# Performance work log

Measured on AMD Instinct MI355X. Metric: run time of the kernel, lower is better.

The kernel has to match this reference:

```python
import jax, jax.numpy as jnp
import numpy as np


def setup_inputs() -> dict:
    key = jax.random.key(0)
    k1, k2 = jax.random.split(key)
    B, Lc, Lm, D = 8, 2048, 2048, 128
    context = jax.random.normal(k1, (B, Lc, D), dtype=jnp.float32)
    main = jax.random.normal(k2, (B, Lm, D), dtype=jnp.float32)
    return {"context": context, "main": main}


def reference(context, main):
    # weights[b,c,m] = sum_d context[b,c,d] * main[b,m,d]   (Keras dot axes=[2,2])
    weights = jnp.einsum("bcd,bmd->bcm", context, main)
    # K.softmax default axis=-1: normalize over the main-length axis m
    weights = jax.nn.softmax(weights, axis=-1)
    # dot([weights, context], axes=1): contract axis 1 (c) of both -> (B, Lm, D)
    weighted = jnp.einsum("bcm,bcd->bmd", weights, context)
    return main - weighted
```

## Files before the change

### kernel.cpp

```cpp
#include <hip/hip_runtime.h>


#define BATCH 8
#define L_SEQ 2048
#define DD 128
#define SHIFT 40.0f
#define LDA 136

typedef __attribute__((ext_vector_type(8))) short bf16x8;
typedef __attribute__((ext_vector_type(4))) short bf16x4;
typedef __attribute__((ext_vector_type(4))) float f32x4;
typedef __attribute__((ext_vector_type(16))) float f32x16;
typedef __attribute__((ext_vector_type(4))) unsigned int uint4v;

__device__ __forceinline__ short f2bf(float f) {
    unsigned u = __builtin_bit_cast(unsigned, f);
    return (short)((u + 0x8000u) >> 16);
}

__device__ __forceinline__ void gl2lds16(const short* g, short* l) {
    __builtin_amdgcn_global_load_lds(
        (const __attribute__((address_space(1))) unsigned int*)g,
        (__attribute__((address_space(3))) unsigned int*)l, 16, 0, 0);
}

__device__ __forceinline__ void waitv8() { asm volatile("s_waitcnt vmcnt(8)" ::: "memory"); }
__device__ __forceinline__ void waitv4() { asm volatile("s_waitcnt vmcnt(4)" ::: "memory"); }
__device__ __forceinline__ void waitv0() { asm volatile("s_waitcnt vmcnt(0)" ::: "memory"); }

template <int NT>
__device__ __forceinline__ void stage_tile(short* __restrict__ dst,
                                           const float* __restrict__ src,
                                           int nelts, int t) {
    for (int base = 0; base < nelts; base += NT * 8) {
        int flat = base + t * 8;
        const float4* p = (const float4*)(src + flat);
        float4 v0 = p[0];
        float4 v1 = p[1];
        bf16x8 s;
        s[0] = f2bf(v0.x); s[1] = f2bf(v0.y); s[2] = f2bf(v0.z); s[3] = f2bf(v0.w);
        s[4] = f2bf(v1.x); s[5] = f2bf(v1.y); s[6] = f2bf(v1.z); s[7] = f2bf(v1.w);
        int row = flat >> 7;
        int col = flat & 127;
        *(bf16x8*)&dst[row * LDA + col] = s;
    }
}

__global__ __launch_bounds__(256) void zero_kernel(float* __restrict__ p, int n) {
    int i = blockIdx.x * 256 + threadIdx.x;
    if (i < n) p[i] = 0.0f;
}


__global__ __launch_bounds__(256) void convert_kernel(const float* __restrict__ ctx,
                                                      const float* __restrict__ mn,
                                                      short* __restrict__ Cbf,
                                                      short* __restrict__ Mbf,
                                                      float* __restrict__ Lg) {
    int tid = blockIdx.x * 256 + threadIdx.x;
    if (tid < BATCH * L_SEQ) Lg[tid] = 0.0f;
    const int half = BATCH * L_SEQ * DD / 8;
    int id = tid;
    const float* src;
    short* dst;
    if (id < half) { src = ctx; dst = Cbf; }
    else           { id -= half; src = mn; dst = Mbf; }
    int row = id >> 4;
    int lc = id & 15;
    const float4* p = (const float4*)(src + ((size_t)row << 7) + lc * 8);
    float4 v0 = p[0];
    float4 v1 = p[1];
    bf16x8 s;
    s[0] = f2bf(v0.x); s[1] = f2bf(v0.y); s[2] = f2bf(v0.z); s[3] = f2bf(v0.w);
    s[4] = f2bf(v1.x); s[5] = f2bf(v1.y); s[6] = f2bf(v1.z); s[7] = f2bf(v1.w);
    int pc = (lc & 8) | ((lc ^ row) & 7);
    *(bf16x8*)&dst[((size_t)row << 7) + pc * 8] = s;
}

__global__ __launch_bounds__(256, 2) void stats_kernel(const short* __restrict__ Cbf,
                                                       const short* __restrict__ Mbf,
                                                       float* __restrict__ Lg) {
    __shared__ short Cs[128 * 128];
    __shared__ short Ms[2][64 * 128];

    int bid = blockIdx.x;
    int b  = bid & 7;
    int r2 = bid >> 3;
    int mc = r2 & 3;
    int ct = r2 >> 2;
    int t = threadIdx.x;
    int w = t >> 6;
    int l = t & 63;
    int a15 = l & 15;
    int q = l >> 4;
    int h = a15 & 7;
    int cw = (w & 1) * 64;
    int mw = (w >> 1) * 32;

    const short* gC = Cbf + ((size_t)(b * L_SEQ + ct * 128)) * DD;
    const short* gM = Mbf + ((size_t)(b * L_SEQ + mc * 512)) * DD;

    {
        #pragma unroll
        for (int ii = 0; ii < 8; ++ii) {
            int inst = w * 8 + ii;
            gl2lds16(gC + inst * 512 + l * 8, Cs + inst * 512);
        }
        #pragma unroll
        for (int ii = 0; ii < 4; ++ii) {
            int inst = w * 4 + ii;
            gl2lds16(gM + inst * 512 + l * 8, Ms[0] + inst * 512);
        }
        #pragma unroll
        for (int ii = 0; ii < 4; ++ii) {
            int inst = w * 4 + ii;
            gl2lds16(gM + (size_t)64 * DD + inst * 512 + l * 8, Ms[1] + inst * 512);
        }
    }

    waitv8();
    __builtin_amdgcn_s_barrier();
    __builtin_amdgcn_sched_barrier(0);

    bf16x8 af[4][4];
    #pragma unroll
    for (int ks = 0; ks < 4; ++ks) {
        int aoff = ((ks * 4 + q) ^ h) * 8;
        #pragma unroll
        for (int i = 0; i < 4; ++i)
            af[ks][i] = *(const bf16x8*)&Cs[(cw + i * 16 + a15) * 128 + aoff];
    }

    float ls[4][4] = {};

    for (int ms = 0; ms < 8; ++ms) {
        int bp = ms & 1;
        if (ms < 7) waitv4(); else waitv0();
        __builtin_amdgcn_s_barrier();
        __builtin_amdgcn_sched_barrier(0);

        f32x4 acc[4][2];
        #pragma unroll
        for (int i = 0; i < 4; ++i)
            #pragma unroll
            for (int j = 0; j < 2; ++j) {
                f32x4 z = {0.f, 0.f, 0.f, 0.f};
                acc[i][j] = z;
            }
        #pragma unroll
        for (int ks = 0; ks < 4; ++ks) {
            int aoff = ((ks * 4 + q) ^ h) * 8;
            bf16x8 bv[2];
            #pragma unroll
            for (int j = 0; j < 2; ++j)
                bv[j] = *(const bf16x8*)&Ms[bp][(mw + j * 16 + a15) * 128 + aoff];
            #pragma unroll
            for (int i = 0; i < 4; ++i)
                #pragma unroll
                for (int j = 0; j < 2; ++j)
                    acc[i][j] = __builtin_amdgcn_mfma_f32_16x16x32_bf16(af[ks][i], bv[j], acc[i][j], 0, 0, 0);
        }

        #pragma unroll
        for (int j = 0; j < 2; ++j)
            #pragma unroll
            for (int i = 0; i < 4; ++i)
                #pragma unroll
                for (int r = 0; r < 4; ++r)
                    ls[i][r] += __expf(acc[i][j][r] - SHIFT);

        __builtin_amdgcn_s_barrier();
        __builtin_amdgcn_sched_barrier(0);
        if (ms + 2 < 8) {
            #pragma unroll
            for (int ii = 0; ii < 4; ++ii) {
                int inst = w * 4 + ii;
                gl2lds16(gM + (size_t)(ms + 2) * 64 * DD + inst * 512 + l * 8,
                         Ms[bp] + inst * 512);
            }
        }
    }

    #pragma unroll
    for (int i = 0; i < 4; ++i)
        #pragma unroll
        for (int r = 0; r < 4; ++r) {
            float v = ls[i][r];
            v += __shfl_xor(v, 1);
            v += __shfl_xor(v, 2);
            v += __shfl_xor(v, 4);
            v += __shfl_xor(v, 8);
            ls[i][r] = v;
        }
    if (a15 == 0) {
        #pragma unroll
        for (int i = 0; i < 4; ++i) {
            int c = ct * 128 + cw + i * 16 + q * 4;
            #pragma unroll
            for (int r = 0; r < 4; ++r)
                atomicAdd(&Lg[(size_t)b * L_SEQ + c + r], ls[i][r]);
        }
    }
}

__global__ __launch_bounds__(256) void prep_kernel(const float* __restrict__ ctx,
                                                   const float* __restrict__ Lg,
                                                   short* __restrict__ CtLf) {
    __shared__ short Ts[128 * LDA];
    __shared__ float invLs[128];

    int b = blockIdx.x >> 4;
    int cc = blockIdx.x & 15;
    int t = threadIdx.x;

    if (t < 128) invLs[t] = 1.0f / Lg[(size_t)b * L_SEQ + cc * 128 + t];
    __syncthreads();

    const float* src = ctx + ((size_t)(b * L_SEQ + cc * 128)) * DD;
    #pragma unroll
    for (int i = 0; i < 8; ++i) {
        int flat = i * 2048 + t * 8;
        int r = flat >> 7;
        int c = flat & 127;
        const float4* p = (const float4*)(src + flat);
        float4 v0 = p[0];
        float4 v1 = p[1];
        float il = invLs[r];
        bf16x8 s;
        s[0] = f2bf(v0.x * il); s[1] = f2bf(v0.y * il); s[2] = f2bf(v0.z * il); s[3] = f2bf(v0.w * il);
        s[4] = f2bf(v1.x * il); s[5] = f2bf(v1.y * il); s[6] = f2bf(v1.z * il); s[7] = f2bf(v1.w * il);
        *(bf16x8*)&Ts[r * LDA + c] = s;
    }
    __syncthreads();

    #pragma unroll
    for (int i = 0; i < 8; ++i) {
        int slot = i * 256 + t;
        int rec = slot >> 6;
        int l2  = slot & 63;
        int chh = rec >> 3;
        int dgg = (rec >> 1) & 3;
        int ks2 = rec & 1;
        int la2 = l2 & 31;
        int hi2 = l2 >> 5;
        int d   = dgg * 32 + la2;
        int c0  = (chh * 4 + ks2 * 2 + hi2) * 8;
        bf16x8 v;
        #pragma unroll
        for (int j = 0; j < 8; ++j) v[j] = Ts[(c0 + j) * LDA + d];
        *(bf16x8*)&CtLf[((size_t)(b * 16 + cc) * 32 + rec) * 512 + l2 * 8] = v;
    }
}

__global__ __launch_bounds__(256, 2) void attend_fused(const short* __restrict__ Cbf,
                                                       const short* __restrict__ Mbf,
                                                       const short* __restrict__ CtLf,
                                                       const float* __restrict__ mn,
                                                       float* __restrict__ out) {
    __shared__ __align__(16) char smem[65536];

    int bid = blockIdx.x;
    int b = bid & 7;
    int mtile = bid >> 3;
    int t = threadIdx.x;
    int w = t >> 6;
    int l = t & 63;
    int la = l & 31;
    int hi = l >> 5;
    int ch = w;

    int m_glob = mtile * 32 + la;
    int key7 = la & 7;

    bf16x8 mf[8];
    {
        const short* mrow = Mbf + ((size_t)(b * L_SEQ + m_glob)) * DD;
        #pragma unroll
        for (int ks = 0; ks < 8; ++ks) {
            int lc = ks * 2 + hi;
            int pc = (lc & 8) | ((lc ^ key7) & 7);
            mf[ks] = *(const bf16x8*)&mrow[pc * 8];
        }
    }

    auto stage = [&](int cs, int p) {
        short* Cw = (short*)(smem + p * 32768);
        const short* gC = Cbf + ((size_t)(b * L_SEQ + cs * 128)) * DD;
        #pragma unroll
        for (int ii = 0; ii < 8; ++ii) {
            int inst = w * 8 + ii;
            gl2lds16(gC + inst * 512 + l * 8, Cw + inst * 512);
        }
    };

    f32x16 o[4];
    #pragma unroll
    for (int dg = 0; dg < 4; ++dg)
        #pragma unroll
        for (int r = 0; r < 16; ++r) o[dg][r] = 0.0f;

    stage(0, 0);
    stage(1, 1);

    for (int cs = 0; cs < 16; ++cs) {
        int p = cs & 1;
        waitv8();
        __builtin_amdgcn_s_barrier();
        __builtin_amdgcn_sched_barrier(0);

        const short* gF = CtLf + ((size_t)((b * 16 + cs) * 4 + ch) * 8) * 512 + l * 8;
        bf16x8 tv[4][2];
        #pragma unroll
        for (int dg = 0; dg < 4; ++dg)
            #pragma unroll
            for (int ks2 = 0; ks2 < 2; ++ks2)
                tv[dg][ks2] = *(const bf16x8*)&gF[(dg * 2 + ks2) * 512];

        const short* Cw = (const short*)(smem + p * 32768);

        f32x16 s;
        #pragma unroll
        for (int r = 0; r < 16; ++r) s[r] = 0.0f;
        int crow = ch * 32 + la;
        #pragma unroll
        for (int ks = 0; ks < 8; ++ks) {
            int lc = ks * 2 + hi;
            int pc = (lc & 8) | ((lc ^ key7) & 7);
            bf16x8 av = *(const bf16x8*)&Cw[crow * 128 + pc * 8];
            s = __builtin_amdgcn_mfma_f32_32x32x16_bf16(av, mf[ks], s, 0, 0, 0);
        }

        unsigned u[4][2];
        #pragma unroll
        for (int q = 0; q < 4; ++q)
            #pragma unroll
            for (int jj = 0; jj < 2; ++jj) {
                float e0 = __expf(s[q * 4 + jj * 2]     - SHIFT);
                float e1 = __expf(s[q * 4 + jj * 2 + 1] - SHIFT);
                u[q][jj] = ((unsigned)(unsigned short)f2bf(e1) << 16)
                         |  (unsigned)(unsigned short)f2bf(e0);
            }

        bf16x8 pa[2];
        #pragma unroll
        for (int ks2 = 0; ks2 < 2; ++ks2) {
            unsigned a0 = u[2 * ks2][0],     a1 = u[2 * ks2][1];
            unsigned b0 = u[2 * ks2 + 1][0], b1 = u[2 * ks2 + 1][1];
            unsigned a0p = (unsigned)__shfl_xor((int)a0, 32);
            unsigned a1p = (unsigned)__shfl_xor((int)a1, 32);
            unsigned b0p = (unsigned)__shfl_xor((int)b0, 32);
            unsigned b1p = (unsigned)__shfl_xor((int)b1, 32);
            uint4v pw;
            pw.x = hi ? b0p : a0;
            pw.y = hi ? b1p : a1;
            pw.z = hi ? b0  : a0p;
            pw.w = hi ? b1  : a1p;
            pa[ks2] = __builtin_bit_cast(bf16x8, pw);
        }

        #pragma unroll
        for (int dg = 0; dg < 4; ++dg)
            #pragma unroll
            for (int ks2 = 0; ks2 < 2; ++ks2)
                o[dg] = __builtin_amdgcn_mfma_f32_32x32x16_bf16(tv[dg][ks2], pa[ks2], o[dg], 0, 0, 0);

        __builtin_amdgcn_s_barrier();
        __builtin_amdgcn_sched_barrier(0);
        if (cs + 2 < 16) stage(cs + 2, p);
    }

    __syncthreads();
    float* red = (float*)smem;
    {
        float* base = red + w * 4096;
        #pragma unroll
        for (int dg = 0; dg < 4; ++dg)
            #pragma unroll
            for (int r = 0; r < 16; ++r) {
                int d = dg * 32 + (r & 3) + 8 * (r >> 2) + 4 * hi;
                base[d * 32 + la] = o[dg][r];
            }
    }
    __syncthreads();

    {
        int m  = t & 31;
        int dq = t >> 5;
        size_t gbase = ((size_t)(b * L_SEQ + mtile * 32 + m)) * DD + dq * 16;
        #pragma unroll
        for (int jq = 0; jq < 4; ++jq) {
            f32x4 v;
            #pragma unroll
            for (int e = 0; e < 4; ++e) {
                int idx = (dq * 16 + jq * 4 + e) * 32 + m;
                v[e] = red[idx] + red[4096 + idx] + red[8192 + idx] + red[12288 + idx];
            }
            f32x4 mv = *(const f32x4*)&mn[gbase + jq * 4];
            f32x4 ov;
            ov[0] = mv[0] - v[0]; ov[1] = mv[1] - v[1];
            ov[2] = mv[2] - v[2]; ov[3] = mv[3] - v[3];
            *(f32x4*)&out[gbase + jq * 4] = ov;
        }
    }
}


__global__ __launch_bounds__(256, 4) void stats_fb(const float* __restrict__ ctx,
                                                   const float* __restrict__ mn,
                                                   float* __restrict__ Lg) {
    __shared__ short Cs[64 * LDA];
    __shared__ short Ms[64 * LDA];

    int bid = blockIdx.x;
    int mc = bid & 3;
    int ct = (bid >> 2) & 31;
    int b  = bid >> 7;
    int t = threadIdx.x;
    int w = t >> 6;
    int l = t & 63;
    int a15 = l & 15;
    int q = l >> 4;

    stage_tile<256>(Cs, ctx + ((size_t)b * L_SEQ + ct * 64) * DD, 64 * DD, t);

    float ls[4] = {0.f, 0.f, 0.f, 0.f};
    for (int mt = 0; mt < 8; ++mt) {
        __syncthreads();
        int m0 = (mc * 8 + mt) * 64;
        stage_tile<256>(Ms, mn + ((size_t)b * L_SEQ + m0) * DD, 64 * DD, t);
        __syncthreads();

        f32x4 acc[4] = {{0.f,0.f,0.f,0.f},{0.f,0.f,0.f,0.f},{0.f,0.f,0.f,0.f},{0.f,0.f,0.f,0.f}};
        #pragma unroll
        for (int ks = 0; ks < 4; ++ks) {
            int k0 = ks * 32 + q * 8;
            bf16x8 a = *(const bf16x8*)&Cs[(w * 16 + a15) * LDA + k0];
            #pragma unroll
            for (int g = 0; g < 4; ++g) {
                bf16x8 bb = *(const bf16x8*)&Ms[(g * 16 + a15) * LDA + k0];
                acc[g] = __builtin_amdgcn_mfma_f32_16x16x32_bf16(a, bb, acc[g], 0, 0, 0);
            }
        }
        #pragma unroll
        for (int g = 0; g < 4; ++g)
            #pragma unroll
            for (int r = 0; r < 4; ++r)
                ls[r] += __expf(acc[g][r] - SHIFT);
    }

    #pragma unroll
    for (int r = 0; r < 4; ++r) {
        float v = ls[r];
        v += __shfl_xor(v, 1);
        v += __shfl_xor(v, 2);
        v += __shfl_xor(v, 4);
        v += __shfl_xor(v, 8);
        ls[r] = v;
    }
    if (a15 == 0) {
        int c = ct * 64 + w * 16 + q * 4;
        #pragma unroll
        for (int r = 0; r < 4; ++r)
            atomicAdd(&Lg[(size_t)b * L_SEQ + c + r], ls[r]);
    }
}

__global__ __launch_bounds__(1024, 4) void attend_fb(const float* __restrict__ ctx,
                                                     const float* __restrict__ mn,
                                                     const float* __restrict__ Lg,
                                                     float* __restrict__ out) {
    __shared__ short Mt[64 * LDA];
    __shared__ short Cs[128 * LDA];
    __shared__ short Ct[128 * LDA];
    __shared__ short Ps[64 * LDA];
    __shared__ float invLs[128];

    int bid = blockIdx.x;
    int mtile = bid & 31;
    int b = bid >> 5;
    int m0 = mtile * 64;
    int t = threadIdx.x;
    int w = t >> 6;
    int l = t & 63;
    int a15 = l & 15;
    int q = l >> 4;
    int mg = w & 3;
    int pg = w >> 2;

    stage_tile<1024>(Mt, mn + ((size_t)b * L_SEQ + m0) * DD, 64 * DD, t);

    f32x4 oacc[2] = {{0.f,0.f,0.f,0.f},{0.f,0.f,0.f,0.f}};

    for (int cs = 0; cs < 16; ++cs) {
        int c0 = cs * 128;
        __syncthreads();
        stage_tile<1024>(Cs, ctx + ((size_t)b * L_SEQ + c0) * DD, 128 * DD, t);
        if (t < 128) invLs[t] = 1.0f / Lg[(size_t)b * L_SEQ + c0 + t];
        __syncthreads();

        {
            int cc = t & 127;
            int d0 = (t >> 7) * 16;
            #pragma unroll
            for (int hh = 0; hh < 2; ++hh) {
                bf16x8 v = *(const bf16x8*)&Cs[cc * LDA + d0 + hh * 8];
                #pragma unroll
                for (int j = 0; j < 8; ++j)
                    Ct[(d0 + hh * 8 + j) * LDA + cc] = v[j];
            }
        }

        f32x4 sacc[2] = {{0.f,0.f,0.f,0.f},{0.f,0.f,0.f,0.f}};
        #pragma unroll
        for (int ks = 0; ks < 4; ++ks) {
            int k0 = ks * 32 + q * 8;
            bf16x8 a = *(const bf16x8*)&Mt[(mg * 16 + a15) * LDA + k0];
            #pragma unroll
            for (int g = 0; g < 2; ++g) {
                bf16x8 bb = *(const bf16x8*)&Cs[((pg * 2 + g) * 16 + a15) * LDA + k0];
                sacc[g] = __builtin_amdgcn_mfma_f32_16x16x32_bf16(a, bb, sacc[g], 0, 0, 0);
            }
        }
        #pragma unroll
        for (int g = 0; g < 2; ++g) {
            int cl = (pg * 2 + g) * 16 + a15;
            float il = invLs[cl];
            #pragma unroll
            for (int r = 0; r < 4; ++r) {
                float p = __expf(sacc[g][r] - SHIFT) * il;
                Ps[(mg * 16 + q * 4 + r) * LDA + cl] = f2bf(p);
            }
        }
        __syncthreads();

        #pragma unroll
        for (int ks = 0; ks < 4; ++ks) {
            int k0 = ks * 32 + q * 8;
            bf16x8 a = *(const bf16x8*)&Ps[(mg * 16 + a15) * LDA + k0];
            #pragma unroll
            for (int g = 0; g < 2; ++g) {
                bf16x8 bb = *(const bf16x8*)&Ct[((pg * 2 + g) * 16 + a15) * LDA + k0];
                oacc[g] = __builtin_amdgcn_mfma_f32_16x16x32_bf16(a, bb, oacc[g], 0, 0, 0);
            }
        }
    }

    #pragma unroll
    for (int g = 0; g < 2; ++g) {
        int dl = (pg * 2 + g) * 16 + a15;
        #pragma unroll
        for (int r = 0; r < 4; ++r) {
            int ml = mg * 16 + q * 4 + r;
            size_t idx = ((size_t)b * L_SEQ + m0 + ml) * DD + dl;
            out[idx] = mn[idx] - oacc[g][r];
        }
    }
}


extern "C" void kernel_launch(void* const* d_in, const int* in_sizes, int n_in,
                              void* d_out, int out_size, void* d_ws, size_t ws_size,
                              hipStream_t stream) {
    const float* ctx = (const float*)d_in[0];
    const float* mn  = (const float*)d_in[1];
    float* out = (float*)d_out;

    const size_t LG_BYTES = (size_t)BATCH * L_SEQ * sizeof(float);
    const size_t BF_BYTES = (size_t)BATCH * L_SEQ * DD * sizeof(short);
    const size_t NEED = LG_BYTES + 3 * BF_BYTES;

    float* Lg = (float*)d_ws;

    if (ws_size >= NEED) {
        short* Cbf  = (short*)((char*)d_ws + LG_BYTES);
        short* Mbf  = (short*)((char*)d_ws + LG_BYTES + BF_BYTES);
        short* CtLf = (short*)((char*)d_ws + LG_BYTES + 2 * BF_BYTES);
        convert_kernel<<<2048, 256, 0, stream>>>(ctx, mn, Cbf, Mbf, Lg);
        stats_kernel<<<BATCH * 16 * 4, 256, 0, stream>>>(Cbf, Mbf, Lg);
        prep_kernel<<<BATCH * 16, 256, 0, stream>>>(ctx, Lg, CtLf);
        attend_fused<<<BATCH * 64, 256, 0, stream>>>(Cbf, Mbf, CtLf, mn, out);
    } else {
        int nL = BATCH * L_SEQ;
        zero_kernel<<<(nL + 255) / 256, 256, 0, stream>>>(Lg, nL);
        stats_fb<<<BATCH * 32 * 4, 256, 0, stream>>>(ctx, mn, Lg);
        attend_fb<<<BATCH * 32, 1024, 0, stream>>>(ctx, mn, Lg, out);
    }
}
```

Baseline: 121.2 us.

## Fuse convert, stats, prep and attend into one cooperative kernel with grid syncs

Replaces the four separate launches with a single cooperative mega-kernel of 512 blocks that runs the conversion, log-sum statistics, scaled-context prep and attention phases, separated by grid.sync(). The aim is to remove the kernel launch gaps and tail effects between stages. The trade-offs are grid-wide barrier cost, a fixed 512-block grid that loses the parallelism shapes of the original stages (for example, conversion now loops four times per thread), and 64KB of LDS per block under launch_bounds(256,2). If the cooperative launch fails, it falls back to the old four-kernel path.

```diff
diff --git a/kernel.cpp b/kernel.cpp
--- a/kernel.cpp
+++ b/kernel.cpp
@@ -1,4 +1,7 @@
 #include <hip/hip_runtime.h>
+#include <hip/hip_cooperative_groups.h>
+
+namespace cg = cooperative_groups;
 
 
 #define BATCH 8
@@ -49,6 +52,361 @@
 __global__ __launch_bounds__(256) void zero_kernel(float* __restrict__ p, int n) {
     int i = blockIdx.x * 256 + threadIdx.x;
     if (i < n) p[i] = 0.0f;
+}
+
+
+__global__ __launch_bounds__(256, 2) void mega_kernel(const float* __restrict__ ctx,
+                                                      const float* __restrict__ mn,
+                                                      short* __restrict__ Cbf,
+                                                      short* __restrict__ Mbf,
+                                                      short* __restrict__ CtLf,
+                                                      float* __restrict__ Lg,
+                                                      float* __restrict__ out) {
+    __shared__ __align__(16) char smem[65536];
+    cg::grid_group grid = cg::this_grid();
+
+    int bid = blockIdx.x;
+    int t = threadIdx.x;
+    int w = t >> 6;
+    int l = t & 63;
+    int b = bid & 7;
+
+    {
+        int tid = bid * 256 + t;
+        if (tid < BATCH * L_SEQ) Lg[tid] = 0.0f;
+        const int half = BATCH * L_SEQ * DD / 8;
+        #pragma unroll
+        for (int k = 0; k < 4; ++k) {
+            int id = tid + k * 131072;
+            const float* src;
+            short* dst;
+            if (id < half) { src = ctx; dst = Cbf; }
+            else           { id -= half; src = mn; dst = Mbf; }
+            int row = id >> 4;
+            int lc = id & 15;
+            const float4* p = (const float4*)(src + ((size_t)row << 7) + lc * 8);
+            float4 v0 = p[0];
+            float4 v1 = p[1];
+            bf16x8 s;
+            s[0] = f2bf(v0.x); s[1] = f2bf(v0.y); s[2] = f2bf(v0.z); s[3] = f2bf(v0.w);
+            s[4] = f2bf(v1.x); s[5] = f2bf(v1.y); s[6] = f2bf(v1.z); s[7] = f2bf(v1.w);
+            int pc = (lc & 8) | ((lc ^ row) & 7);
+            *(bf16x8*)&dst[((size_t)row << 7) + pc * 8] = s;
+        }
+    }
+
+    grid.sync();
+
+    {
+        short* Cs = (short*)smem;
+
+        int r2 = bid >> 3;
+        int mc = r2 & 3;
+        int ct = r2 >> 2;
+        int a15 = l & 15;
+        int q = l >> 4;
+        int h = a15 & 7;
+        int cw = (w & 1) * 64;
+        int mw = (w >> 1) * 32;
+
+        const short* gC = Cbf + ((size_t)(b * L_SEQ + ct * 128)) * DD;
+        const short* gM = Mbf + ((size_t)(b * L_SEQ + mc * 512)) * DD;
+
+        #pragma unroll
+        for (int ii = 0; ii < 8; ++ii) {
+            int inst = w * 8 + ii;
+            gl2lds16(gC + inst * 512 + l * 8, Cs + inst * 512);
+        }
+        #pragma unroll
+        for (int ii = 0; ii < 4; ++ii) {
+            int inst = w * 4 + ii;
+            gl2lds16(gM + inst * 512 + l * 8, (short*)(smem + 32768) + inst * 512);
+        }
+        #pragma unroll
+        for (int ii = 0; ii < 4; ++ii) {
+            int inst = w * 4 + ii;
+            gl2lds16(gM + (size_t)64 * DD + inst * 512 + l * 8,
+                     (short*)(smem + 49152) + inst * 512);
+        }
+
+        waitv8();
+        __builtin_amdgcn_s_barrier();
+        __builtin_amdgcn_sched_barrier(0);
+
+        bf16x8 af[4][4];
+        #pragma unroll
+        for (int ks = 0; ks < 4; ++ks) {
+            int aoff = ((ks * 4 + q) ^ h) * 8;
+            #pragma unroll
+            for (int i = 0; i < 4; ++i)
+                af[ks][i] = *(const bf16x8*)&Cs[(cw + i * 16 + a15) * 128 + aoff];
+        }
+
+        float ls[4][4] = {};
+
+        for (int ms = 0; ms < 8; ++ms) {
+            int bp = ms & 1;
+            short* Msb = (short*)(smem + 32768 + bp * 16384);
+            if (ms < 7) waitv4(); else waitv0();
+            __builtin_amdgcn_s_barrier();
+            __builtin_amdgcn_sched_barrier(0);
+
+            f32x4 acc[4][2];
+            #pragma unroll
+            for (int i = 0; i < 4; ++i)
+                #pragma unroll
+                for (int j = 0; j < 2; ++j) {
+                    f32x4 z = {0.f, 0.f, 0.f, 0.f};
+                    acc[i][j] = z;
+                }
+            #pragma unroll
+            for (int ks = 0; ks < 4; ++ks) {
+                int aoff = ((ks * 4 + q) ^ h) * 8;
+                bf16x8 bv[2];
+                #pragma unroll
+                for (int j = 0; j < 2; ++j)
+                    bv[j] = *(const bf16x8*)&Msb[(mw + j * 16 + a15) * 128 + aoff];
+                #pragma unroll
+                for (int i = 0; i < 4; ++i)
+                    #pragma unroll
+                    for (int j = 0; j < 2; ++j)
+                        acc[i][j] = __builtin_amdgcn_mfma_f32_16x16x32_bf16(af[ks][i], bv[j], acc[i][j], 0, 0, 0);
+            }
+
+            #pragma unroll
+            for (int j = 0; j < 2; ++j)
+                #pragma unroll
+                for (int i = 0; i < 4; ++i)
+                    #pragma unroll
+                    for (int r = 0; r < 4; ++r)
+                        ls[i][r] += __expf(acc[i][j][r] - SHIFT);
+
+            __builtin_amdgcn_s_barrier();
+            __builtin_amdgcn_sched_barrier(0);
+            if (ms + 2 < 8) {
+                #pragma unroll
+                for (int ii = 0; ii < 4; ++ii) {
+                    int inst = w * 4 + ii;
+                    gl2lds16(gM + (size_t)(ms + 2) * 64 * DD + inst * 512 + l * 8,
+                             Msb + inst * 512);
+                }
+            }
+        }
+
+        #pragma unroll
+        for (int i = 0; i < 4; ++i)
+            #pragma unroll
+            for (int r = 0; r < 4; ++r) {
+                float v = ls[i][r];
+                v += __shfl_xor(v, 1);
+                v += __shfl_xor(v, 2);
+                v += __shfl_xor(v, 4);
+                v += __shfl_xor(v, 8);
+                ls[i][r] = v;
+            }
+        if (a15 == 0) {
+            #pragma unroll
+            for (int i = 0; i < 4; ++i) {
+                int c = ct * 128 + cw + i * 16 + q * 4;
+                #pragma unroll
+                for (int r = 0; r < 4; ++r)
+                    atomicAdd(&Lg[(size_t)b * L_SEQ + c + r], ls[i][r]);
+            }
+        }
+    }
+
+    grid.sync();
+
+    {
+        short* Ts = (short*)smem;
+        float* invL = (float*)(smem + 8704);
+
+        int j = bid >> 3;
+        int cc = j >> 2;
+        int qq = j & 3;
+
+        if (t < 32) invL[t] = 1.0f / Lg[(size_t)b * L_SEQ + cc * 128 + qq * 32 + t];
+        __syncthreads();
+
+        const float* src = ctx + ((size_t)(b * L_SEQ + cc * 128 + qq * 32)) * DD;
+        #pragma unroll
+        for (int i = 0; i < 2; ++i) {
+            int flat = i * 2048 + t * 8;
+            int r = flat >> 7;
+            int c = flat & 127;
+            const float4* p = (const float4*)(src + flat);
+            float4 v0 = p[0];
+            float4 v1 = p[1];
+            float il = invL[r];
+            bf16x8 s;
+            s[0] = f2bf(v0.x * il); s[1] = f2bf(v0.y * il); s[2] = f2bf(v0.z * il); s[3] = f2bf(v0.w * il);
+            s[4] = f2bf(v1.x * il); s[5] = f2bf(v1.y * il); s[6] = f2bf(v1.z * il); s[7] = f2bf(v1.w * il);
+            *(bf16x8*)&Ts[r * LDA + c] = s;
+        }
+        __syncthreads();
+
+        #pragma unroll
+        for (int i = 0; i < 2; ++i) {
+            int slot = i * 256 + t;
+            int recl = slot >> 6;
+            int l2  = slot & 63;
+            int dgg = recl >> 1;
+            int ks2 = recl & 1;
+            int la2 = l2 & 31;
+            int hi2 = l2 >> 5;
+            int d   = dgg * 32 + la2;
+            int rb  = (ks2 * 2 + hi2) * 8;
+            bf16x8 v;
+            #pragma unroll
+            for (int jj = 0; jj < 8; ++jj) v[jj] = Ts[(rb + jj) * LDA + d];
+            int rec = qq * 8 + recl;
+            *(bf16x8*)&CtLf[((size_t)(b * 16 + cc) * 32 + rec) * 512 + l2 * 8] = v;
+        }
+        __syncthreads();
+    }
+
+    grid.sync();
+
+    {
+        int mtile = bid >> 3;
+        int la = l & 31;
+        int hi = l >> 5;
+        int ch = w;
+
+        int m_glob = mtile * 32 + la;
+        int key7 = la & 7;
+
+        bf16x8 mf[8];
+        {
+            const short* mrow = Mbf + ((size_t)(b * L_SEQ + m_glob)) * DD;
+            #pragma unroll
+            for (int ks = 0; ks < 8; ++ks) {
+                int lc = ks * 2 + hi;
+                int pc = (lc & 8) | ((lc ^ key7) & 7);
+                mf[ks] = *(const bf16x8*)&mrow[pc * 8];
+            }
+        }
+
+        auto stage = [&](int cs, int p) {
+            short* Cw = (short*)(smem + p * 32768);
+            const short* gC = Cbf + ((size_t)(b * L_SEQ + cs * 128)) * DD;
+            #pragma unroll
+            for (int ii = 0; ii < 8; ++ii) {
+                int inst = w * 8 + ii;
+                gl2lds16(gC + inst * 512 + l * 8, Cw + inst * 512);
+            }
+        };
+
+        f32x16 o[4];
+        #pragma unroll
+        for (int dg = 0; dg < 4; ++dg)
+            #pragma unroll
+            for (int r = 0; r < 16; ++r) o[dg][r] = 0.0f;
+
+        stage(0, 0);
+        stage(1, 1);
+
+        for (int cs = 0; cs < 16; ++cs) {
+            int p = cs & 1;
+            waitv8();
+            __builtin_amdgcn_s_barrier();
+            __builtin_amdgcn_sched_barrier(0);
+
+            const short* gF = CtLf + ((size_t)((b * 16 + cs) * 4 + ch) * 8) * 512 + l * 8;
+            bf16x8 tv[4][2];
+            #pragma unroll
+            for (int dg = 0; dg < 4; ++dg)
+                #pragma unroll
+                for (int ks2 = 0; ks2 < 2; ++ks2)
+                    tv[dg][ks2] = *(const bf16x8*)&gF[(dg * 2 + ks2) * 512];
+
+            const short* Cw = (const short*)(smem + p * 32768);
+
+            f32x16 s;
+            #pragma unroll
+            for (int r = 0; r < 16; ++r) s[r] = 0.0f;
+            int crow = ch * 32 + la;
+            #pragma unroll
+            for (int ks = 0; ks < 8; ++ks) {
+                int lc = ks * 2 + hi;
+                int pc = (lc & 8) | ((lc ^ key7) & 7);
+                bf16x8 av = *(const bf16x8*)&Cw[crow * 128 + pc * 8];
+                s = __builtin_amdgcn_mfma_f32_32x32x16_bf16(av, mf[ks], s, 0, 0, 0);
+            }
+
+            unsigned u[4][2];
+            #pragma unroll
+            for (int q = 0; q < 4; ++q)
+                #pragma unroll
+                for (int jj = 0; jj < 2; ++jj) {
+                    float e0 = __expf(s[q * 4 + jj * 2]     - SHIFT);
+                    float e1 = __expf(s[q * 4 + jj * 2 + 1] - SHIFT);
+                    u[q][jj] = ((unsigned)(unsigned short)f2bf(e1) << 16)
+                             |  (unsigned)(unsigned short)f2bf(e0);
+                }
+
+            bf16x8 pa[2];
+            #pragma unroll
+            for (int ks2 = 0; ks2 < 2; ++ks2) {
+                unsigned a0 = u[2 * ks2][0],     a1 = u[2 * ks2][1];
+                unsigned b0 = u[2 * ks2 + 1][0], b1 = u[2 * ks2 + 1][1];
+                unsigned a0p = (unsigned)__shfl_xor((int)a0, 32);
+                unsigned a1p = (unsigned)__shfl_xor((int)a1, 32);
+                unsigned b0p = (unsigned)__shfl_xor((int)b0, 32);
+                unsigned b1p = (unsigned)__shfl_xor((int)b1, 32);
+                uint4v pw;
+                pw.x = hi ? b0p : a0;
+                pw.y = hi ? b1p : a1;
+                pw.z = hi ? b0  : a0p;
+                pw.w = hi ? b1  : a1p;
+                pa[ks2] = __builtin_bit_cast(bf16x8, pw);
+            }
+
+            #pragma unroll
+            for (int dg = 0; dg < 4; ++dg)
+                #pragma unroll
+                for (int ks2 = 0; ks2 < 2; ++ks2)
+                    o[dg] = __builtin_amdgcn_mfma_f32_32x32x16_bf16(tv[dg][ks2], pa[ks2], o[dg], 0, 0, 0);
+
+            __builtin_amdgcn_s_barrier();
+            __builtin_amdgcn_sched_barrier(0);
+            if (cs + 2 < 16) stage(cs + 2, p);
+        }
+
+        __syncthreads();
+        float* red = (float*)smem;
+        {
+            float* base = red + w * 4096;
+            #pragma unroll
+            for (int dg = 0; dg < 4; ++dg)
+                #pragma unroll
+                for (int r = 0; r < 16; ++r) {
+                    int d = dg * 32 + (r & 3) + 8 * (r >> 2) + 4 * hi;
+                    base[d * 32 + la] = o[dg][r];
+                }
+        }
+        __syncthreads();
+
+        {
+            int m  = t & 31;
+            int dq = t >> 5;
+            size_t gbase = ((size_t)(b * L_SEQ + mtile * 32 + m)) * DD + dq * 16;
+            #pragma unroll
+            for (int jq = 0; jq < 4; ++jq) {
+                f32x4 v;
+                #pragma unroll
+                for (int e = 0; e < 4; ++e) {
+                    int idx = (dq * 16 + jq * 4 + e) * 32 + m;
+                    v[e] = red[idx] + red[4096 + idx] + red[8192 + idx] + red[12288 + idx];
+                }
+                f32x4 mv = *(const f32x4*)&mn[gbase + jq * 4];
+                f32x4 ov;
+                ov[0] = mv[0] - v[0]; ov[1] = mv[1] - v[1];
+                ov[2] = mv[2] - v[2]; ov[3] = mv[3] - v[3];
+                *(f32x4*)&out[gbase + jq * 4] = ov;
+            }
+        }
+    }
 }
 
 
@@ -100,22 +458,20 @@
     const short* gC = Cbf + ((size_t)(b * L_SEQ + ct * 128)) * DD;
     const short* gM = Mbf + ((size_t)(b * L_SEQ + mc * 512)) * DD;
 
-    {
-        #pragma unroll
-        for (int ii = 0; ii < 8; ++ii) {
-            int inst = w * 8 + ii;
-            gl2lds16(gC + inst * 512 + l * 8, Cs + inst * 512);
-        }
-        #pragma unroll
-        for (int ii = 0; ii < 4; ++ii) {
-            int inst = w * 4 + ii;
-            gl2lds16(gM + inst * 512 + l * 8, Ms[0] + inst * 512);
-        }
-        #pragma unroll
-        for (int ii = 0; ii < 4; ++ii) {
-            int inst = w * 4 + ii;
-            gl2lds16(gM + (size_t)64 * DD + inst * 512 + l * 8, Ms[1] + inst * 512);
-        }
+    #pragma unroll
+    for (int ii = 0; ii < 8; ++ii) {
+        int inst = w * 8 + ii;
+        gl2lds16(gC + inst * 512 + l * 8, Cs + inst * 512);
+    }
+    #pragma unroll
+    for (int ii = 0; ii < 4; ++ii) {
+        int inst = w * 4 + ii;
+        gl2lds16(gM + inst * 512 + l * 8, Ms[0] + inst * 512);
+    }
+    #pragma unroll
+    for (int ii = 0; ii < 4; ++ii) {
+        int inst = w * 4 + ii;
+        gl2lds16(gM + (size_t)64 * DD + inst * 512 + l * 8, Ms[1] + inst * 512);
     }
 
     waitv8();
@@ -575,10 +931,18 @@
         short* Cbf  = (short*)((char*)d_ws + LG_BYTES);
         short* Mbf  = (short*)((char*)d_ws + LG_BYTES + BF_BYTES);
         short* CtLf = (short*)((char*)d_ws + LG_BYTES + 2 * BF_BYTES);
-        convert_kernel<<<2048, 256, 0, stream>>>(ctx, mn, Cbf, Mbf, Lg);
-        stats_kernel<<<BATCH * 16 * 4, 256, 0, stream>>>(Cbf, Mbf, Lg);
-        prep_kernel<<<BATCH * 16, 256, 0, stream>>>(ctx, Lg, CtLf);
-        attend_fused<<<BATCH * 64, 256, 0, stream>>>(Cbf, Mbf, CtLf, mn, out);
+
+        void* args[] = {(void*)&ctx, (void*)&mn, (void*)&Cbf, (void*)&Mbf,
+                        (void*)&CtLf, (void*)&Lg, (void*)&out};
+        hipError_t err = hipLaunchCooperativeKernel(
+            reinterpret_cast<void*>(mega_kernel), dim3(512), dim3(256),
+            args, 0, stream);
+        if (err != hipSuccess) {
+            convert_kernel<<<2048, 256, 0, stream>>>(ctx, mn, Cbf, Mbf, Lg);
+            stats_kernel<<<BATCH * 16 * 4, 256, 0, stream>>>(Cbf, Mbf, Lg);
+            prep_kernel<<<BATCH * 16, 256, 0, stream>>>(ctx, Lg, CtLf);
+            attend_fused<<<BATCH * 64, 256, 0, stream>>>(Cbf, Mbf, CtLf, mn, out);
+        }
     } else {
         int nL = BATCH * L_SEQ;
         zero_kernel<<<(nL + 255) / 256, 256, 0, stream>>>(Lg, nL);
```

New measurement: 279.4 us. 131% more time.
